# Performance work log

Hardware: AMD Instinct MI355X
Metric: run time of the kernel (lower is better)

## Reference

```python
import jax, jax.numpy as jnp
from jax import lax
import numpy as np

P, K1, K2 = 8, 5, 9  # nPaths, small/large ECA kernel sizes (from nDim=1024, nPaths=8)
LN_EPS = 1e-5


def setup_inputs() -> dict:
    key = jax.random.key(0)
    ks = jax.random.split(key, 6)
    b, c, l = 16, 1024, 4096
    return {
        "x": jax.random.normal(ks[0], (b, c, l), dtype=jnp.float32),
        "conv1_w": jax.random.normal(ks[1], (P, K1), dtype=jnp.float32) * 0.3,
        "conv2_w": jax.random.normal(ks[2], (P, K2), dtype=jnp.float32) * 0.3,
        "combine_w": jax.random.normal(ks[3], (2,), dtype=jnp.float32) * 0.5,
        "combine_b": jnp.zeros((), dtype=jnp.float32),
        "ln_g": jnp.ones((P,), dtype=jnp.float32),
        "ln_b": jnp.zeros((P,), dtype=jnp.float32),
        "W1": jax.random.normal(ks[4], (P, 2 * P), dtype=jnp.float32) * 0.3,
        "b1": jnp.zeros((2 * P,), dtype=jnp.float32),
        "W2": jax.random.normal(ks[5], (2 * P, P), dtype=jnp.float32) * 0.3,
        "b2": jnp.zeros((P,), dtype=jnp.float32),
    }


def _grouped_conv(y, w):
    # y: (b, P, D) pooled per-path features; w: (P, k) one 1-ch kernel per path.
    # Equivalent to the per-path Conv1d(1,1,k, padding=(k-1)//2) loop, fused.
    k = w.shape[-1]
    pad = (k - 1) // 2
    return lax.conv_general_dilated(
        y, w[:, None, :], window_strides=(1,), padding=[(pad, pad)],
        dimension_numbers=("NCH", "OIH", "NCH"), feature_group_count=y.shape[1])


def reference(x, conv1_w, conv2_w, combine_w, combine_b, ln_g, ln_b, W1, b1, W2, b2):
    b, c, l = x.shape
    nP = conv1_w.shape[0]
    D = c // nP
    pf = x.reshape(b, nP, D, l)          # (b, P, D, l)
    y = pf.mean(-1)                      # (b, P, D) global-avg-pool over l
    y1 = _grouped_conv(y, conv1_w)       # (b, P, D)
    y2 = _grouped_conv(y, conv2_w)       # (b, P, D)
    # combine = Conv1d(2,1,1): scalar mix of the two conv outputs + bias
    attn = jax.nn.sigmoid(combine_w[0] * y1 + combine_w[1] * y2 + combine_b)
    # cross-path gating MLP on per-path mean attention
    cross = attn.mean(-1)                # (b, P)
    mu = cross.mean(-1, keepdims=True)
    var = cross.var(-1, keepdims=True)   # biased, matches torch LayerNorm
    h = (cross - mu) / jnp.sqrt(var + LN_EPS) * ln_g + ln_b
    h = jax.nn.gelu(h @ W1 + b1, approximate=False)
    gate = jax.nn.sigmoid(h @ W2 + b2)   # (b, P)
    scale = attn * gate[:, :, None]      # (b, P, D)
    out = pf * scale[..., None]          # broadcast over l
    return out.reshape(b, c, l)
```

## Files before the change

kernel.cpp:

```cpp
#include <hip/hip_runtime.h>
#include <hip/hip_cooperative_groups.h>
#include <math.h>

namespace cg = cooperative_groups;

#define NP 8
#define ND 128
#define NC 1024
#define NL 4096
#define NB 16
#define LN_EPS 1e-5f

#define NBLK 2048
#define RPB 8

typedef float v4f __attribute__((ext_vector_type(4)));

__device__ __forceinline__ void attn_math(const float* __restrict__ sy,
                                          float* __restrict__ sattn,
                                          const float* conv1_w, const float* conv2_w,
                                          const float* combine_w, const float* combine_b,
                                          int tid) {
    #pragma unroll
    for (int k = 0; k < 4; ++k) {
        const int pos = tid + 256 * k;
        const int p = pos >> 7, d = pos & 127;
        const float* rowp = sy + p * ND;
        float c1 = 0.f;
        #pragma unroll
        for (int t = 0; t < 5; ++t) {
            int dd = d + t - 2;
            float v = (dd >= 0 && dd < ND) ? rowp[dd] : 0.f;
            c1 += conv1_w[p * 5 + t] * v;
        }
        float c2 = 0.f;
        #pragma unroll
        for (int t = 0; t < 9; ++t) {
            int dd = d + t - 4;
            float v = (dd >= 0 && dd < ND) ? rowp[dd] : 0.f;
            c2 += conv2_w[p * 9 + t] * v;
        }
        const float z = combine_w[0] * c1 + combine_w[1] * c2 + combine_b[0];
        sattn[pos] = 1.f / (1.f + expf(-z));
    }
}

__device__ __forceinline__ void gate_math(const float* __restrict__ scross,
                                          float* __restrict__ sgate,
                                          const float* ln_g, const float* ln_b,
                                          const float* W1, const float* b1,
                                          const float* W2, const float* b2) {
    float cross[NP];
    #pragma unroll
    for (int pp = 0; pp < NP; ++pp) cross[pp] = scross[pp];
    float mu = 0.f;
    #pragma unroll
    for (int pp = 0; pp < NP; ++pp) mu += cross[pp];
    mu *= (1.f / NP);
    float var = 0.f;
    #pragma unroll
    for (int pp = 0; pp < NP; ++pp) { float dl = cross[pp] - mu; var += dl * dl; }
    var *= (1.f / NP);
    const float inv = rsqrtf(var + LN_EPS);
    float h[NP];
    #pragma unroll
    for (int pp = 0; pp < NP; ++pp)
        h[pp] = (cross[pp] - mu) * inv * ln_g[pp] + ln_b[pp];
    float h2[2 * NP];
    for (int j = 0; j < 2 * NP; ++j) {
        float s = b1[j];
        #pragma unroll
        for (int pp = 0; pp < NP; ++pp) s += h[pp] * W1[pp * (2 * NP) + j];
        h2[j] = 0.5f * s * (1.f + erff(s * 0.70710678118654752f));
    }
    for (int pp = 0; pp < NP; ++pp) {
        float s = b2[pp];
        #pragma unroll
        for (int j = 0; j < 2 * NP; ++j) s += h2[j] * W2[j * NP + pp];
        sgate[pp] = 1.f / (1.f + expf(-s));
    }
}

__global__ __launch_bounds__(256, 8) void fused_kernel(
    const float* __restrict__ x, float* __restrict__ y,
    const float* __restrict__ conv1_w, const float* __restrict__ conv2_w,
    const float* __restrict__ combine_w, const float* __restrict__ combine_b,
    const float* __restrict__ ln_g, const float* __restrict__ ln_b,
    const float* __restrict__ W1, const float* __restrict__ b1,
    const float* __restrict__ W2, const float* __restrict__ b2,
    float* __restrict__ out)
{
    const int tid  = threadIdx.x;
    const int row0 = blockIdx.x * RPB;
    const int b    = row0 >> 10;
    const int p0   = (row0 & (NC - 1)) >> 7;

    __shared__ float sred[RPB][4];
    __shared__ float sy[NC];
    __shared__ float sattn[NC];
    __shared__ float scross[NP];
    __shared__ float sgate[NP];

    v4f xd[RPB][4];
    const v4f* xb = (const v4f*)x + (size_t)row0 * (NL / 4);
    v4f* ob       = (v4f*)out    + (size_t)row0 * (NL / 4);

    #pragma unroll
    for (int r = 0; r < RPB; ++r) {
        float ps = 0.f;
        #pragma unroll
        for (int k = 0; k < 4; ++k) {
            xd[r][k] = xb[(size_t)r * (NL / 4) + tid + 256 * k];
            ps += xd[r][k].x + xd[r][k].y + xd[r][k].z + xd[r][k].w;
        }
        #pragma unroll
        for (int off = 32; off; off >>= 1) ps += __shfl_down(ps, off, 64);
        if ((tid & 63) == 0) sred[r][tid >> 6] = ps;
    }
    __syncthreads();
    if (tid < RPB)
        y[row0 + tid] = (sred[tid][0] + sred[tid][1] + sred[tid][2] + sred[tid][3]) * (1.f / NL);
    __threadfence();
    cg::this_grid().sync();

    #pragma unroll
    for (int k = 0; k < 4; ++k) sy[tid + 256 * k] = y[b * NC + tid + 256 * k];
    __syncthreads();
    attn_math(sy, sattn, conv1_w, conv2_w, combine_w, combine_b, tid);
    __syncthreads();
    if (tid < NP) {
        float s = 0.f;
        for (int d = 0; d < ND; ++d) s += sattn[tid * ND + d];
        scross[tid] = s * (1.f / ND);
    }
    __syncthreads();
    if (tid == 0) gate_math(scross, sgate, ln_g, ln_b, W1, b1, W2, b2);
    __syncthreads();

    const float g = sgate[p0];
    #pragma unroll
    for (int r = 0; r < RPB; ++r) {
        const float s = sattn[(row0 & (NC - 1)) + r] * g;
        #pragma unroll
        for (int k = 0; k < 4; ++k) {
            v4f v = xd[r][k] * s;
            __builtin_nontemporal_store(v, &ob[(size_t)r * (NL / 4) + tid + 256 * k]);
        }
    }
}

__global__ __launch_bounds__(256) void pool_kernel(const float* __restrict__ x,
                                                   float* __restrict__ y) {
    const int wid  = threadIdx.x >> 6;
    const int lane = threadIdx.x & 63;
    const int row  = blockIdx.x * 4 + wid;
    const v4f* xr = (const v4f*)(x + (size_t)row * NL);
    float s = 0.f;
    #pragma unroll
    for (int i = 0; i < 16; ++i) {
        v4f v = xr[lane + i * 64];
        s += v.x + v.y + v.z + v.w;
    }
    #pragma unroll
    for (int off = 32; off; off >>= 1) s += __shfl_down(s, off, 64);
    if (lane == 0) y[row] = s * (1.f / NL);
}

__global__ __launch_bounds__(1024) void attn_kernel(
    const float* __restrict__ y,
    const float* __restrict__ conv1_w, const float* __restrict__ conv2_w,
    const float* __restrict__ combine_w, const float* __restrict__ combine_b,
    const float* __restrict__ ln_g, const float* __restrict__ ln_b,
    const float* __restrict__ W1, const float* __restrict__ b1,
    const float* __restrict__ W2, const float* __restrict__ b2,
    float* __restrict__ scale)
{
    const int b = blockIdx.x;
    const int tid = threadIdx.x;
    const int p = tid >> 7;
    const int d = tid & 127;

    __shared__ float sy[NC];
    __shared__ float sattn[NC];
    __shared__ float sred[16];
    __shared__ float sgate[NP];

    sy[tid] = y[b * NC + tid];
    __syncthreads();

    const float* rowp = sy + p * ND;
    float c1 = 0.f;
    #pragma unroll
    for (int t = 0; t < 5; ++t) {
        int dd = d + t - 2;
        float v = (dd >= 0 && dd < ND) ? rowp[dd] : 0.f;
        c1 += conv1_w[p * 5 + t] * v;
    }
    float c2 = 0.f;
    #pragma unroll
    for (int t = 0; t < 9; ++t) {
        int dd = d + t - 4;
        float v = (dd >= 0 && dd < ND) ? rowp[dd] : 0.f;
        c2 += conv2_w[p * 9 + t] * v;
    }
    const float z = combine_w[0] * c1 + combine_w[1] * c2 + combine_b[0];
    const float a = 1.f / (1.f + expf(-z));
    sattn[tid] = a;

    float r = a;
    #pragma unroll
    for (int off = 32; off; off >>= 1) r += __shfl_down(r, off, 64);
    const int lane = tid & 63, wid = tid >> 6;
    if (lane == 0) sred[wid] = r;
    __syncthreads();

    if (tid == 0) {
        float scross[NP];
        #pragma unroll
        for (int pp = 0; pp < NP; ++pp)
            scross[pp] = (sred[2 * pp] + sred[2 * pp + 1]) * (1.f / ND);
        gate_math(scross, sgate, ln_g, ln_b, W1, b1, W2, b2);
    }
    __syncthreads();

    scale[b * NC + tid] = sattn[tid] * sgate[p];
}

__global__ __launch_bounds__(256) void scale_kernel(const float* __restrict__ x,
                                                    const float* __restrict__ scale,
                                                    float* __restrict__ out) {
    const v4f* xv = (const v4f*)x;
    v4f* ov = (v4f*)out;
    const size_t n = (size_t)NB * NC * (NL / 4);
    const size_t stride = (size_t)gridDim.x * blockDim.x;
    for (size_t i = (size_t)blockIdx.x * blockDim.x + threadIdx.x; i < n; i += stride) {
        const float s = scale[i >> 10];
        v4f v = xv[i];
        v *= s;
        __builtin_nontemporal_store(v, &ov[i]);
    }
}

extern "C" void kernel_launch(void* const* d_in, const int* in_sizes, int n_in,
                              void* d_out, int out_size, void* d_ws, size_t ws_size,
                              hipStream_t stream) {
    const float* x         = (const float*)d_in[0];
    const float* conv1_w   = (const float*)d_in[1];
    const float* conv2_w   = (const float*)d_in[2];
    const float* combine_w = (const float*)d_in[3];
    const float* combine_b = (const float*)d_in[4];
    const float* ln_g      = (const float*)d_in[5];
    const float* ln_b      = (const float*)d_in[6];
    const float* W1        = (const float*)d_in[7];
    const float* b1        = (const float*)d_in[8];
    const float* W2        = (const float*)d_in[9];
    const float* b2        = (const float*)d_in[10];
    float* out = (float*)d_out;

    float* y     = (float*)d_ws;
    float* scale = y + NB * NC;

    int nb = 0;
    hipOccupancyMaxActiveBlocksPerMultiprocessor(&nb, fused_kernel, 256, 0);
    if (nb >= NBLK / 256) {
        void* args[] = { (void*)&x, (void*)&y,
                         (void*)&conv1_w, (void*)&conv2_w,
                         (void*)&combine_w, (void*)&combine_b,
                         (void*)&ln_g, (void*)&ln_b,
                         (void*)&W1, (void*)&b1, (void*)&W2, (void*)&b2,
                         (void*)&out };
        hipLaunchCooperativeKernel((const void*)fused_kernel, dim3(NBLK), dim3(256),
                                   args, 0, stream);
    } else {
        pool_kernel<<<NB * NC / 4, 256, 0, stream>>>(x, y);
        attn_kernel<<<NB, 1024, 0, stream>>>(y, conv1_w, conv2_w, combine_w, combine_b,
                                             ln_g, ln_b, W1, b1, W2, b2, scale);
        scale_kernel<<<2048, 256, 0, stream>>>(x, scale, out);
    }
}
```

Measured before the change: 133.3 us.

## Replace cooperative grid sync with atomic counter barrier and scalarized row registers

Replaces the cooperative-groups grid sync with a hand-rolled barrier in which each block atomically increments a global counter that is zeroed by a memset before launch. Thread 0 then spins with s_sleep until all blocks have arrived. The per-row register array becomes macro-expanded scalar variables to avoid indexed-array spills, the per-path attention mean becomes a parallel shuffle reduction, and exact erf GELU is replaced with the tanh approximation. The custom barrier still relies on every block being co-resident and adds a memset launch, and the tanh GELU changes numerics slightly.

Result: slower. 137.1 us (+2.8%).

```diff
diff --git a/kernel.cpp b/kernel.cpp
--- a/kernel.cpp
+++ b/kernel.cpp
@@ -1,8 +1,5 @@
 #include <hip/hip_runtime.h>
-#include <hip/hip_cooperative_groups.h>
 #include <math.h>
-
-namespace cg = cooperative_groups;
 
 #define NP 8
 #define ND 128
@@ -15,6 +12,50 @@
 #define RPB 8
 
 typedef float v4f __attribute__((ext_vector_type(4)));
+
+__device__ __forceinline__ float hsum(v4f v) { return v.x + v.y + v.z + v.w; }
+
+__device__ __forceinline__ float gelu_f(float s) {
+    const float t = 0.7978845608028654f * (s + 0.044715f * s * s * s);
+    const float e = expf(2.f * t);
+    return 0.5f * s * (1.f + (e - 1.f) / (e + 1.f));
+}
+
+__device__ __forceinline__ void gate_math(const float* __restrict__ scross,
+                                          float* __restrict__ sgate,
+                                          const float* ln_g, const float* ln_b,
+                                          const float* W1, const float* b1,
+                                          const float* W2, const float* b2) {
+    float cross[NP];
+    #pragma unroll
+    for (int pp = 0; pp < NP; ++pp) cross[pp] = scross[pp];
+    float mu = 0.f;
+    #pragma unroll
+    for (int pp = 0; pp < NP; ++pp) mu += cross[pp];
+    mu *= (1.f / NP);
+    float var = 0.f;
+    #pragma unroll
+    for (int pp = 0; pp < NP; ++pp) { float dl = cross[pp] - mu; var += dl * dl; }
+    var *= (1.f / NP);
+    const float inv = rsqrtf(var + LN_EPS);
+    float h[NP];
+    #pragma unroll
+    for (int pp = 0; pp < NP; ++pp)
+        h[pp] = (cross[pp] - mu) * inv * ln_g[pp] + ln_b[pp];
+    float h2[2 * NP];
+    for (int j = 0; j < 2 * NP; ++j) {
+        float s = b1[j];
+        #pragma unroll
+        for (int pp = 0; pp < NP; ++pp) s += h[pp] * W1[pp * (2 * NP) + j];
+        h2[j] = gelu_f(s);
+    }
+    for (int pp = 0; pp < NP; ++pp) {
+        float s = b2[pp];
+        #pragma unroll
+        for (int j = 0; j < 2 * NP; ++j) s += h2[j] * W2[j * NP + pp];
+        sgate[pp] = 1.f / (1.f + expf(-s));
+    }
+}
 
 __device__ __forceinline__ void attn_math(const float* __restrict__ sy,
                                           float* __restrict__ sattn,
@@ -45,44 +86,26 @@
     }
 }
 
-__device__ __forceinline__ void gate_math(const float* __restrict__ scross,
-                                          float* __restrict__ sgate,
-                                          const float* ln_g, const float* ln_b,
-                                          const float* W1, const float* b1,
-                                          const float* W2, const float* b2) {
-    float cross[NP];
-    #pragma unroll
-    for (int pp = 0; pp < NP; ++pp) cross[pp] = scross[pp];
-    float mu = 0.f;
-    #pragma unroll
-    for (int pp = 0; pp < NP; ++pp) mu += cross[pp];
-    mu *= (1.f / NP);
-    float var = 0.f;
-    #pragma unroll
-    for (int pp = 0; pp < NP; ++pp) { float dl = cross[pp] - mu; var += dl * dl; }
-    var *= (1.f / NP);
-    const float inv = rsqrtf(var + LN_EPS);
-    float h[NP];
-    #pragma unroll
-    for (int pp = 0; pp < NP; ++pp)
-        h[pp] = (cross[pp] - mu) * inv * ln_g[pp] + ln_b[pp];
-    float h2[2 * NP];
-    for (int j = 0; j < 2 * NP; ++j) {
-        float s = b1[j];
-        #pragma unroll
-        for (int pp = 0; pp < NP; ++pp) s += h[pp] * W1[pp * (2 * NP) + j];
-        h2[j] = 0.5f * s * (1.f + erff(s * 0.70710678118654752f));
-    }
-    for (int pp = 0; pp < NP; ++pp) {
-        float s = b2[pp];
-        #pragma unroll
-        for (int j = 0; j < 2 * NP; ++j) s += h2[j] * W2[j * NP + pp];
-        sgate[pp] = 1.f / (1.f + expf(-s));
-    }
-}
+#define DECL_ROW(r) v4f xr##r##_0, xr##r##_1, xr##r##_2, xr##r##_3;
+#define LOAD_ROW(r) { \
+    const v4f* rp = xb + (size_t)(r) * (NL / 4); \
+    xr##r##_0 = rp[tid]; xr##r##_1 = rp[tid + 256]; \
+    xr##r##_2 = rp[tid + 512]; xr##r##_3 = rp[tid + 768]; \
+    float ps = hsum(xr##r##_0) + hsum(xr##r##_1) + hsum(xr##r##_2) + hsum(xr##r##_3); \
+    ps += __shfl_down(ps, 32, 64); ps += __shfl_down(ps, 16, 64); \
+    ps += __shfl_down(ps, 8, 64);  ps += __shfl_down(ps, 4, 64); \
+    ps += __shfl_down(ps, 2, 64);  ps += __shfl_down(ps, 1, 64); \
+    if ((tid & 63) == 0) sred[r][tid >> 6] = ps; }
+#define STORE_ROW(r) { \
+    const float s = sattn[cbase + (r)] * g; \
+    v4f* op = ob + (size_t)(r) * (NL / 4); \
+    __builtin_nontemporal_store(xr##r##_0 * s, &op[tid]); \
+    __builtin_nontemporal_store(xr##r##_1 * s, &op[tid + 256]); \
+    __builtin_nontemporal_store(xr##r##_2 * s, &op[tid + 512]); \
+    __builtin_nontemporal_store(xr##r##_3 * s, &op[tid + 768]); }
 
 __global__ __launch_bounds__(256, 8) void fused_kernel(
-    const float* __restrict__ x, float* __restrict__ y,
+    const float* __restrict__ x, float* __restrict__ y, unsigned* __restrict__ cnt,
     const float* __restrict__ conv1_w, const float* __restrict__ conv2_w,
     const float* __restrict__ combine_w, const float* __restrict__ combine_b,
     const float* __restrict__ ln_g, const float* __restrict__ ln_b,
@@ -90,10 +113,11 @@
     const float* __restrict__ W2, const float* __restrict__ b2,
     float* __restrict__ out)
 {
-    const int tid  = threadIdx.x;
-    const int row0 = blockIdx.x * RPB;
-    const int b    = row0 >> 10;
-    const int p0   = (row0 & (NC - 1)) >> 7;
+    const int tid   = threadIdx.x;
+    const int row0  = blockIdx.x * RPB;
+    const int b     = row0 >> 10;
+    const int cbase = row0 & (NC - 1);
+    const int p0    = cbase >> 7;
 
     __shared__ float sred[RPB][4];
     __shared__ float sy[NC];
@@ -101,52 +125,51 @@
     __shared__ float scross[NP];
     __shared__ float sgate[NP];
 
-    v4f xd[RPB][4];
     const v4f* xb = (const v4f*)x + (size_t)row0 * (NL / 4);
     v4f* ob       = (v4f*)out    + (size_t)row0 * (NL / 4);
 
-    #pragma unroll
-    for (int r = 0; r < RPB; ++r) {
-        float ps = 0.f;
-        #pragma unroll
-        for (int k = 0; k < 4; ++k) {
-            xd[r][k] = xb[(size_t)r * (NL / 4) + tid + 256 * k];
-            ps += xd[r][k].x + xd[r][k].y + xd[r][k].z + xd[r][k].w;
-        }
-        #pragma unroll
-        for (int off = 32; off; off >>= 1) ps += __shfl_down(ps, off, 64);
-        if ((tid & 63) == 0) sred[r][tid >> 6] = ps;
-    }
+    DECL_ROW(0) DECL_ROW(1) DECL_ROW(2) DECL_ROW(3)
+    DECL_ROW(4) DECL_ROW(5) DECL_ROW(6) DECL_ROW(7)
+
+    LOAD_ROW(0) LOAD_ROW(1) LOAD_ROW(2) LOAD_ROW(3)
+    LOAD_ROW(4) LOAD_ROW(5) LOAD_ROW(6) LOAD_ROW(7)
     __syncthreads();
     if (tid < RPB)
         y[row0 + tid] = (sred[tid][0] + sred[tid][1] + sred[tid][2] + sred[tid][3]) * (1.f / NL);
     __threadfence();
-    cg::this_grid().sync();
-
-    #pragma unroll
-    for (int k = 0; k < 4; ++k) sy[tid + 256 * k] = y[b * NC + tid + 256 * k];
+    __syncthreads();
+
+    if (tid == 0) {
+        __hip_atomic_fetch_add(cnt, 1u, __ATOMIC_RELEASE, __HIP_MEMORY_SCOPE_AGENT);
+        while (__hip_atomic_load(cnt, __ATOMIC_ACQUIRE, __HIP_MEMORY_SCOPE_AGENT) < (unsigned)NBLK)
+            __builtin_amdgcn_s_sleep(2);
+    }
+    __syncthreads();
+
+    #pragma unroll
+    for (int k = 0; k < 4; ++k) {
+        const int i = tid + 256 * k;
+        sy[i] = __hip_atomic_load(&y[b * NC + i], __ATOMIC_RELAXED, __HIP_MEMORY_SCOPE_AGENT);
+    }
     __syncthreads();
     attn_math(sy, sattn, conv1_w, conv2_w, combine_w, combine_b, tid);
     __syncthreads();
-    if (tid < NP) {
+    if (tid < 128) {
+        const int p = tid >> 4, o = (tid & 15) * 8;
         float s = 0.f;
-        for (int d = 0; d < ND; ++d) s += sattn[tid * ND + d];
-        scross[tid] = s * (1.f / ND);
+        #pragma unroll
+        for (int j = 0; j < 8; ++j) s += sattn[p * ND + o + j];
+        s += __shfl_down(s, 8, 16); s += __shfl_down(s, 4, 16);
+        s += __shfl_down(s, 2, 16); s += __shfl_down(s, 1, 16);
+        if ((tid & 15) == 0) scross[p] = s * (1.f / ND);
     }
     __syncthreads();
     if (tid == 0) gate_math(scross, sgate, ln_g, ln_b, W1, b1, W2, b2);
     __syncthreads();
 
     const float g = sgate[p0];
-    #pragma unroll
-    for (int r = 0; r < RPB; ++r) {
-        const float s = sattn[(row0 & (NC - 1)) + r] * g;
-        #pragma unroll
-        for (int k = 0; k < 4; ++k) {
-            v4f v = xd[r][k] * s;
-            __builtin_nontemporal_store(v, &ob[(size_t)r * (NL / 4) + tid + 256 * k]);
-        }
-    }
+    STORE_ROW(0) STORE_ROW(1) STORE_ROW(2) STORE_ROW(3)
+    STORE_ROW(4) STORE_ROW(5) STORE_ROW(6) STORE_ROW(7)
 }
 
 __global__ __launch_bounds__(256) void pool_kernel(const float* __restrict__ x,
@@ -257,13 +280,16 @@
     const float* b2        = (const float*)d_in[10];
     float* out = (float*)d_out;
 
-    float* y     = (float*)d_ws;
-    float* scale = y + NB * NC;
+    float* y        = (float*)d_ws;
+    float* scale    = y + NB * NC;
+    unsigned* cnt   = (unsigned*)scale;
+
+    hipMemsetAsync((void*)cnt, 0, 64, stream);
 
     int nb = 0;
     hipOccupancyMaxActiveBlocksPerMultiprocessor(&nb, fused_kernel, 256, 0);
     if (nb >= NBLK / 256) {
-        void* args[] = { (void*)&x, (void*)&y,
+        void* args[] = { (void*)&x, (void*)&y, (void*)&cnt,
                          (void*)&conv1_w, (void*)&conv2_w,
                          (void*)&combine_w, (void*)&combine_b,
                          (void*)&ln_g, (void*)&ln_b,
```
